# Kernel tuning notes

Hardware: AMD Instinct MI355X
Metric: run time of the kernel (lower is better)

## Reference

```python
import jax, jax.numpy as jnp
import numpy as np

N_NODES = 100000
N_EDGES = 1600000
F_IN = 64
HIDDEN = 128
N_GRAPHS = 1024
EPS = 1e-5  # BatchNorm1d eps


def setup_inputs() -> dict:
    key = jax.random.key(0)
    ks = jax.random.split(key, 16)
    inp = {
        "x": jax.random.normal(ks[0], (N_NODES, F_IN), jnp.float32),
        "edge_index": jax.random.randint(ks[1], (2, N_EDGES), 0, N_NODES, dtype=jnp.int32),
        "edge_attr": jax.random.uniform(ks[2], (N_EDGES, 1), jnp.float32),
        "batch": jnp.sort(jax.random.randint(ks[3], (N_NODES,), 0, N_GRAPHS, dtype=jnp.int32)),
    }
    dims = [F_IN, HIDDEN, HIDDEN]
    for i in range(3):
        d_in = dims[i]
        kk = jax.random.split(ks[4 + i], 2)
        s = 1.0 / np.sqrt(d_in).astype(np.float32)
        inp[f"rel_w{i}"] = jax.random.uniform(kk[0], (d_in, HIDDEN), jnp.float32, -s, s)
        inp[f"rel_b{i}"] = jnp.zeros((HIDDEN,), jnp.float32)
        inp[f"root_w{i}"] = jax.random.uniform(kk[1], (d_in, HIDDEN), jnp.float32, -s, s)
        inp[f"bn_g{i}"] = jnp.ones((HIDDEN,), jnp.float32)
        inp[f"bn_b{i}"] = jnp.zeros((HIDDEN,), jnp.float32)
        inp[f"bn_m{i}"] = jnp.zeros((HIDDEN,), jnp.float32)
        inp[f"bn_v{i}"] = jnp.ones((HIDDEN,), jnp.float32)
    inp["head_w1"] = jax.random.uniform(ks[8], (HIDDEN, HIDDEN // 2), jnp.float32, -0.1, 0.1)
    inp["head_b1"] = jnp.zeros((HIDDEN // 2,), jnp.float32)
    inp["head_w2"] = jax.random.uniform(ks[9], (HIDDEN // 2, 1), jnp.float32, -0.1, 0.1)
    inp["head_b2"] = jnp.zeros((1,), jnp.float32)
    return inp


def _graph_conv(h, src, dst, ew, w_rel, b_rel, w_root):
    # PyG GraphConv (aggr='add'): lin_rel(sum_j e_ji * x_j) + lin_root(x_i)
    msg = h[src] * ew[:, None]                                   # [E, in] gather
    agg = jax.ops.segment_sum(msg, dst, num_segments=h.shape[0])  # [N, in] scatter-add
    return agg @ w_rel + b_rel + h @ w_root


def reference(x, edge_index, edge_attr, batch,
              rel_w0, rel_b0, root_w0, bn_g0, bn_b0, bn_m0, bn_v0,
              rel_w1, rel_b1, root_w1, bn_g1, bn_b1, bn_m1, bn_v1,
              rel_w2, rel_b2, root_w2, bn_g2, bn_b2, bn_m2, bn_v2,
              head_w1, head_b1, head_w2, head_b2):
    src, dst = edge_index[0], edge_index[1]
    ew = edge_attr[:, 0]
    layers = [
        (rel_w0, rel_b0, root_w0, bn_g0, bn_b0, bn_m0, bn_v0),
        (rel_w1, rel_b1, root_w1, bn_g1, bn_b1, bn_m1, bn_v1),
        (rel_w2, rel_b2, root_w2, bn_g2, bn_b2, bn_m2, bn_v2),
    ]
    h = x
    for (wr, br, wo, g, b, m, v) in layers:
        h = _graph_conv(h, src, dst, ew, wr, br, wo)
        # BatchNorm1d in eval mode (running stats) + ReLU; dropout is identity in eval
        h = jax.nn.relu((h - m) * (g * jax.lax.rsqrt(v + EPS)) + b)
    # global_mean_pool over graph assignment ids
    sums = jax.ops.segment_sum(h, batch, num_segments=N_GRAPHS)                       # [G, H]
    cnts = jax.ops.segment_sum(jnp.ones((h.shape[0],), h.dtype), batch, num_segments=N_GRAPHS)
    pooled = sums / jnp.maximum(cnts, 1.0)[:, None]
    hid = jax.nn.relu(pooled @ head_w1 + head_b1)
    out = hid @ head_w2 + head_b2
    return out[:, 0]
```

## Files before the change

### kernel.cpp

```cpp
#include <hip/hip_runtime.h>

#define N_NODES 100000
#define N_EDGES 1600000
#define F_IN 64
#define HIDDEN 128
#define N_GRAPHS 1024
#define EPS 1e-5f

typedef short short8 __attribute__((ext_vector_type(8)));
typedef float f32x4 __attribute__((ext_vector_type(4)));
typedef unsigned int uint;
typedef unsigned short ushort;

__device__ __forceinline__ ushort f2b(float f) {
    uint x = __float_as_uint(f);
    return (ushort)((x + 0x7fffu + ((x >> 16) & 1u)) >> 16);
}
__device__ __forceinline__ uint pack2(float a, float b) {
    return (uint)f2b(a) | ((uint)f2b(b) << 16);
}
__device__ __forceinline__ float b2f_lo(uint u) { return __uint_as_float(u << 16); }
__device__ __forceinline__ float b2f_hi(uint u) { return __uint_as_float(u & 0xffff0000u); }

#define NBLK_A 128
#define CHUNK ((N_EDGES + NBLK_A - 1) / NBLK_A)
#define BUCK_SHIFT 9
#define NBUCK ((N_NODES + 511) / 512)
#define SCAN_M (NBUCK * NBLK_A)
#define SCAN_T ((SCAN_M + 1023) / 1024)


__global__ __launch_bounds__(256) void bin_count_kernel(const int* __restrict__ ei,
                                                        int* __restrict__ counts) {
    __shared__ int cnt[NBUCK];
    int blk = blockIdx.x, t = threadIdx.x;
    for (int i = t; i < NBUCK; i += 256) cnt[i] = 0;
    __syncthreads();
    int e0 = blk * CHUNK, e1 = min(e0 + CHUNK, N_EDGES);
    for (int e = e0 + t; e < e1; e += 256)
        atomicAdd(&cnt[ei[N_EDGES + e] >> BUCK_SHIFT], 1);
    __syncthreads();
    for (int i = t; i < NBUCK; i += 256) counts[i * NBLK_A + blk] = cnt[i];
}

__global__ __launch_bounds__(1024) void sc_reduce_kernel(const int* __restrict__ counts,
                                                         int* __restrict__ partial) {
    __shared__ int lds[16];
    int b = blockIdx.x, t = threadIdx.x;
    int i = b * 1024 + t;
    int v = (i < SCAN_M) ? counts[i] : 0;
    #pragma unroll
    for (int off = 32; off > 0; off >>= 1) v += __shfl_down(v, off);
    if ((t & 63) == 0) lds[t >> 6] = v;
    __syncthreads();
    if (t == 0) {
        int s = 0;
        #pragma unroll
        for (int j = 0; j < 16; ++j) s += lds[j];
        partial[b] = s;
    }
}

__global__ __launch_bounds__(64) void sc_small_kernel(int* __restrict__ partial,
                                                      int* __restrict__ rowptr) {
    if (threadIdx.x == 0) {
        int s = 0;
        for (int j = 0; j < SCAN_T; ++j) { int v = partial[j]; partial[j] = s; s += v; }
        rowptr[N_NODES] = N_EDGES;
    }
}

__global__ __launch_bounds__(1024) void sc_apply_kernel(int* __restrict__ counts,
                                                        const int* __restrict__ partial) {
    __shared__ int lds[1024];
    int b = blockIdx.x, t = threadIdx.x;
    int i = b * 1024 + t;
    int v = (i < SCAN_M) ? counts[i] : 0;
    lds[t] = v;
    __syncthreads();
    for (int off = 1; off < 1024; off <<= 1) {
        int x = (t >= off) ? lds[t - off] : 0;
        __syncthreads();
        lds[t] += x;
        __syncthreads();
    }
    if (i < SCAN_M) counts[i] = lds[t] - v + partial[b];
}

__global__ __launch_bounds__(256) void bin_scatter_kernel(const int* __restrict__ ei,
                                                          const float* __restrict__ ea,
                                                          const int* __restrict__ counts,
                                                          int2* __restrict__ emb) {
    __shared__ int cur[NBUCK];
    int blk = blockIdx.x, t = threadIdx.x;
    for (int i = t; i < NBUCK; i += 256) cur[i] = counts[i * NBLK_A + blk];
    __syncthreads();
    int e0 = blk * CHUNK, e1 = min(e0 + CHUNK, N_EDGES);
    for (int e = e0 + t; e < e1; e += 256) {
        int s = ei[e], d = ei[N_EDGES + e];
        uint y = ((uint)f2b(ea[e]) << 16) | (uint)(d & 511);
        int p = atomicAdd(&cur[d >> BUCK_SHIFT], 1);
        emb[p] = make_int2(s, (int)y);
    }
}

__global__ __launch_bounds__(1024) void bucket_build_kernel(const int* __restrict__ counts,
                                                            const int2* __restrict__ emb,
                                                            int* __restrict__ rowptr,
                                                            int2* __restrict__ em) {
    __shared__ int hist[512];
    __shared__ int cursor[512];
    int b = blockIdx.x, t = threadIdx.x;
    int beg = counts[b * NBLK_A];
    int end = (b + 1 < NBUCK) ? counts[(b + 1) * NBLK_A] : N_EDGES;
    int nbase = b << BUCK_SHIFT;
    int nnodes = min(512, N_NODES - nbase);

    if (t < 512) hist[t] = 0;
    __syncthreads();
    for (int e = beg + t; e < end; e += 1024)
        atomicAdd(&hist[(uint)emb[e].y & 511u], 1);
    __syncthreads();

    int v = (t < 512) ? hist[t] : 0;
    for (int off = 1; off < 512; off <<= 1) {
        int x = (t < 512 && t >= off) ? hist[t - off] : 0;
        __syncthreads();
        if (t < 512) hist[t] += x;
        __syncthreads();
    }
    if (t < 512) {
        int excl = hist[t] - v;
        cursor[t] = beg + excl;
        if (t < nnodes) rowptr[nbase + t] = beg + excl;
    }
    __syncthreads();

    for (int e = beg + t; e < end; e += 1024) {
        int2 m = emb[e];
        int p = atomicAdd(&cursor[(uint)m.y & 511u], 1);
        em[p] = make_int2(m.x, (int)((uint)m.y & 0xffff0000u));
    }
}


#define PREP_X   (N_NODES * 32)
#define PREP_W0  8192
#define PREP_W1  16384
#define PREP_W2  16384
#define PREP_PZ  (N_GRAPHS * HIDDEN)
#define PREP_TOT (PREP_X + PREP_W0 + PREP_W1 + PREP_W2 + PREP_PZ)

__device__ __forceinline__ void cvt_w_elem(const float* W0, const float* W1, int F,
                                           int idx, uint* out) {
    int K = 2 * F;
    int c  = idx / (K / 2);
    int k2 = (idx % (K / 2)) * 2;
    float f0 = (k2 < F) ? W0[k2 * 128 + c] : W1[(k2 - F) * 128 + c];
    float f1 = (k2 + 1 < F) ? W0[(k2 + 1) * 128 + c] : W1[(k2 + 1 - F) * 128 + c];
    out[idx] = pack2(f0, f1);
}

__global__ __launch_bounds__(256) void prep_kernel(const float* __restrict__ x, uint* __restrict__ xb,
                                                   const float* __restrict__ rw0, const float* __restrict__ ow0,
                                                   const float* __restrict__ rw1, const float* __restrict__ ow1,
                                                   const float* __restrict__ rw2, const float* __restrict__ ow2,
                                                   uint* __restrict__ wb0, uint* __restrict__ wb1,
                                                   uint* __restrict__ wb2, float* __restrict__ pooled) {
    int i = blockIdx.x * 256 + threadIdx.x;
    if (i < PREP_X) {
        float2 v = ((const float2*)x)[i];
        xb[i] = pack2(v.x, v.y);
        return;
    }
    i -= PREP_X;
    if (i < PREP_W0) { cvt_w_elem(rw0, ow0, 64, i, wb0); return; }
    i -= PREP_W0;
    if (i < PREP_W1) { cvt_w_elem(rw1, ow1, 128, i, wb1); return; }
    i -= PREP_W1;
    if (i < PREP_W2) { cvt_w_elem(rw2, ow2, 128, i, wb2); return; }
    i -= PREP_W2;
    if (i < PREP_PZ) pooled[i] = 0.f;
}


template <int F>
__global__ __launch_bounds__(256) void agg_kernel(const ushort* __restrict__ h,
                                                  const int* __restrict__ rowptr,
                                                  const int2* __restrict__ em,
                                                  ushort* __restrict__ agg) {
    int node = blockIdx.x * 4 + (threadIdx.x >> 6);
    int lane = threadIdx.x & 63;
    int g  = lane >> 4;
    int sl = lane & 15;
    int beg = rowptr[node], end = rowptr[node + 1];
    int e = beg;

    if (F == 128) {
        float acc[8] = {};
        for (; e + 8 <= end; e += 8) {
            int2 mA = em[e + g];
            int2 mB = em[e + 4 + g];
            uint4 vA = *(const uint4*)(h + (size_t)mA.x * 128 + sl * 8);
            uint4 vB = *(const uint4*)(h + (size_t)mB.x * 128 + sl * 8);
            float wA = __int_as_float(mA.y), wB = __int_as_float(mB.y);
            acc[0] = fmaf(b2f_lo(vA.x), wA, acc[0]);
            acc[1] = fmaf(b2f_hi(vA.x), wA, acc[1]);
            acc[2] = fmaf(b2f_lo(vA.y), wA, acc[2]);
            acc[3] = fmaf(b2f_hi(vA.y), wA, acc[3]);
            acc[4] = fmaf(b2f_lo(vA.z), wA, acc[4]);
            acc[5] = fmaf(b2f_hi(vA.z), wA, acc[5]);
            acc[6] = fmaf(b2f_lo(vA.w), wA, acc[6]);
            acc[7] = fmaf(b2f_hi(vA.w), wA, acc[7]);
            acc[0] = fmaf(b2f_lo(vB.x), wB, acc[0]);
            acc[1] = fmaf(b2f_hi(vB.x), wB, acc[1]);
            acc[2] = fmaf(b2f_lo(vB.y), wB, acc[2]);
            acc[3] = fmaf(b2f_hi(vB.y), wB, acc[3]);
            acc[4] = fmaf(b2f_lo(vB.z), wB, acc[4]);
            acc[5] = fmaf(b2f_hi(vB.z), wB, acc[5]);
            acc[6] = fmaf(b2f_lo(vB.w), wB, acc[6]);
            acc[7] = fmaf(b2f_hi(vB.w), wB, acc[7]);
        }
        for (; e < end; e += 4) {
            int ej = e + g;
            if (ej < end) {
                int2 m = em[ej];
                uint4 v = *(const uint4*)(h + (size_t)m.x * 128 + sl * 8);
                float w = __int_as_float(m.y);
                acc[0] = fmaf(b2f_lo(v.x), w, acc[0]);
                acc[1] = fmaf(b2f_hi(v.x), w, acc[1]);
                acc[2] = fmaf(b2f_lo(v.y), w, acc[2]);
                acc[3] = fmaf(b2f_hi(v.y), w, acc[3]);
                acc[4] = fmaf(b2f_lo(v.z), w, acc[4]);
                acc[5] = fmaf(b2f_hi(v.z), w, acc[5]);
                acc[6] = fmaf(b2f_lo(v.w), w, acc[6]);
                acc[7] = fmaf(b2f_hi(v.w), w, acc[7]);
            }
        }
        #pragma unroll
        for (int f = 0; f < 8; ++f) {
            acc[f] += __shfl_xor(acc[f], 16);
            acc[f] += __shfl_xor(acc[f], 32);
        }
        if (lane < 16) {
            uint4 o;
            o.x = pack2(acc[0], acc[1]);
            o.y = pack2(acc[2], acc[3]);
            o.z = pack2(acc[4], acc[5]);
            o.w = pack2(acc[6], acc[7]);
            *(uint4*)(agg + (size_t)node * 128 + sl * 8) = o;
        }
    } else {
        float acc[4] = {};
        for (; e + 8 <= end; e += 8) {
            int2 mA = em[e + g];
            int2 mB = em[e + 4 + g];
            uint2 vA = *(const uint2*)(h + (size_t)mA.x * 64 + sl * 4);
            uint2 vB = *(const uint2*)(h + (size_t)mB.x * 64 + sl * 4);
            float wA = __int_as_float(mA.y), wB = __int_as_float(mB.y);
            acc[0] = fmaf(b2f_lo(vA.x), wA, acc[0]);
            acc[1] = fmaf(b2f_hi(vA.x), wA, acc[1]);
            acc[2] = fmaf(b2f_lo(vA.y), wA, acc[2]);
            acc[3] = fmaf(b2f_hi(vA.y), wA, acc[3]);
            acc[0] = fmaf(b2f_lo(vB.x), wB, acc[0]);
            acc[1] = fmaf(b2f_hi(vB.x), wB, acc[1]);
            acc[2] = fmaf(b2f_lo(vB.y), wB, acc[2]);
            acc[3] = fmaf(b2f_hi(vB.y), wB, acc[3]);
        }
        for (; e < end; e += 4) {
            int ej = e + g;
            if (ej < end) {
                int2 m = em[ej];
                uint2 v = *(const uint2*)(h + (size_t)m.x * 64 + sl * 4);
                float w = __int_as_float(m.y);
                acc[0] = fmaf(b2f_lo(v.x), w, acc[0]);
                acc[1] = fmaf(b2f_hi(v.x), w, acc[1]);
                acc[2] = fmaf(b2f_lo(v.y), w, acc[2]);
                acc[3] = fmaf(b2f_hi(v.y), w, acc[3]);
            }
        }
        #pragma unroll
        for (int f = 0; f < 4; ++f) {
            acc[f] += __shfl_xor(acc[f], 16);
            acc[f] += __shfl_xor(acc[f], 32);
        }
        if (lane < 16) {
            uint2 o;
            o.x = pack2(acc[0], acc[1]);
            o.y = pack2(acc[2], acc[3]);
            *(uint2*)(agg + (size_t)node * 64 + sl * 4) = o;
        }
    }
}


template <int F>
__global__ __launch_bounds__(256, 2) void gemm_mfma(const ushort* __restrict__ A0,
                                                    const ushort* __restrict__ A1,
                                                    const ushort* __restrict__ Wb,
                                                    const float* __restrict__ bias,
                                                    const float* __restrict__ bng,
                                                    const float* __restrict__ bnb,
                                                    const float* __restrict__ bnm,
                                                    const float* __restrict__ bnv,
                                                    ushort* __restrict__ out) {
    constexpr int K = 2 * F;
    constexpr int LDW = K + 8;
    __shared__ ushort Wl[128 * LDW];

    int t = threadIdx.x;
    for (int idx = t; idx < 128 * (K / 8); idx += 256) {
        int c  = idx / (K / 8);
        int k8 = (idx % (K / 8)) * 8;
        *(short8*)&Wl[c * LDW + k8] = *(const short8*)&Wb[c * K + k8];
    }
    __syncthreads();

    int wave = t >> 6, lane = t & 63;
    int m = lane & 15, quad = lane >> 4;
    int r0 = blockIdx.x * 128 + wave * 32 + m;
    int r1 = r0 + 16;

    f32x4 acc0[8], acc1[8];
    #pragma unroll
    for (int i = 0; i < 8; ++i) { acc0[i] = (f32x4)(0.f); acc1[i] = (f32x4)(0.f); }

    auto loadA = [&](int row, int k0) -> short8 {
        short8 v = {};
        if (row < N_NODES)
            v = (k0 < F) ? *(const short8*)(A0 + (size_t)row * F + k0)
                         : *(const short8*)(A1 + (size_t)row * F + (k0 - F));
        return v;
    };

    short8 a0 = loadA(r0, quad * 8);
    short8 a1 = loadA(r1, quad * 8);
    for (int kc = 0; kc < K; kc += 32) {
        int k0 = kc + quad * 8;
        short8 na0 = {}, na1 = {};
        if (kc + 32 < K) {
            na0 = loadA(r0, k0 + 32);
            na1 = loadA(r1, k0 + 32);
        }
        #pragma unroll
        for (int ct = 0; ct < 8; ++ct) {
            short8 b = *(const short8*)&Wl[(ct * 16 + m) * LDW + k0];
            acc0[ct] = __builtin_amdgcn_mfma_f32_16x16x32_bf16(a0, b, acc0[ct], 0, 0, 0);
            acc1[ct] = __builtin_amdgcn_mfma_f32_16x16x32_bf16(a1, b, acc1[ct], 0, 0, 0);
        }
        a0 = na0; a1 = na1;
    }

    int rb0 = blockIdx.x * 128 + wave * 32 + quad * 4;
    #pragma unroll
    for (int ct = 0; ct < 8; ++ct) {
        int c = ct * 16 + m;
        float sc = bng[c] * rsqrtf(bnv[c] + EPS);
        float sh = bnb[c] - bnm[c] * sc;
        float bi = bias[c];
        #pragma unroll
        for (int reg = 0; reg < 4; ++reg) {
            int r = rb0 + reg;
            if (r < N_NODES) {
                float v = fmaxf(fmaf(acc0[ct][reg] + bi, sc, sh), 0.f);
                out[(size_t)r * 128 + c] = f2b(v);
            }
            int r2 = rb0 + 16 + reg;
            if (r2 < N_NODES) {
                float v = fmaxf(fmaf(acc1[ct][reg] + bi, sc, sh), 0.f);
                out[(size_t)r2 * 128 + c] = f2b(v);
            }
        }
    }
}


#define POOL_NODES 64
__global__ __launch_bounds__(256) void pool_kernel(const ushort* __restrict__ h,
                                                   const int* __restrict__ batch,
                                                   float* __restrict__ pooled) {
    __shared__ int gb[POOL_NODES];
    int b = blockIdx.x, t = threadIdx.x;
    int n0 = b * POOL_NODES;
    if (t < POOL_NODES) {
        int n = n0 + t;
        gb[t] = (n < N_NODES) ? batch[n] : -1;
    }
    __syncthreads();
    int f2 = t & 63;
    int q  = t >> 6;
    const uint* hp = (const uint*)h;
    float alo = 0.f, ahi = 0.f;
    int gcur = -1;
    for (int i = q; i < POOL_NODES; i += 4) {
        int n = n0 + i;
        if (n >= N_NODES) break;
        int g = gb[i];
        if (g != gcur) {
            if (gcur >= 0) {
                atomicAdd(&pooled[(size_t)gcur * 128 + f2 * 2], alo);
                atomicAdd(&pooled[(size_t)gcur * 128 + f2 * 2 + 1], ahi);
            }
            gcur = g;
            alo = 0.f; ahi = 0.f;
        }
        uint u = hp[(size_t)n * 64 + f2];
        alo += b2f_lo(u);
        ahi += b2f_hi(u);
    }
    if (gcur >= 0) {
        atomicAdd(&pooled[(size_t)gcur * 128 + f2 * 2], alo);
        atomicAdd(&pooled[(size_t)gcur * 128 + f2 * 2 + 1], ahi);
    }
}


__global__ __launch_bounds__(64) void head_kernel(const float* __restrict__ pooled,
                                                  const int* __restrict__ batch,
                                                  const float* __restrict__ w1,
                                                  const float* __restrict__ b1,
                                                  const float* __restrict__ w2,
                                                  const float* __restrict__ b2,
                                                  float* __restrict__ out) {
    int g = blockIdx.x;
    int j = threadIdx.x;
    int lo = 0, hi = N_NODES;
    while (lo < hi) { int m = (lo + hi) >> 1; if (batch[m] <  g) lo = m + 1; else hi = m; }
    int start = lo;
    lo = 0; hi = N_NODES;
    while (lo < hi) { int m = (lo + hi) >> 1; if (batch[m] <= g) lo = m + 1; else hi = m; }
    float inv = 1.0f / fmaxf((float)(lo - start), 1.0f);

    float acc = b1[j];
    #pragma unroll 4
    for (int k = 0; k < 128; ++k)
        acc = fmaf(pooled[(size_t)g * 128 + k] * inv, w1[k * 64 + j], acc);
    float prod = fmaxf(acc, 0.f) * w2[j];
    #pragma unroll
    for (int off = 32; off > 0; off >>= 1)
        prod += __shfl_down(prod, off);
    if (j == 0) out[g] = prod + b2[0];
}


extern "C" void kernel_launch(void* const* d_in, const int* in_sizes, int n_in,
                              void* d_out, int out_size, void* d_ws, size_t ws_size,
                              hipStream_t stream) {
    const float* x     = (const float*)d_in[0];
    const int*   ei    = (const int*)d_in[1];
    const float* ea    = (const float*)d_in[2];
    const int*   batch = (const int*)d_in[3];
    const float* rel_w[3]  = {(const float*)d_in[4],  (const float*)d_in[11], (const float*)d_in[18]};
    const float* rel_b[3]  = {(const float*)d_in[5],  (const float*)d_in[12], (const float*)d_in[19]};
    const float* root_w[3] = {(const float*)d_in[6],  (const float*)d_in[13], (const float*)d_in[20]};
    const float* bn_g[3]   = {(const float*)d_in[7],  (const float*)d_in[14], (const float*)d_in[21]};
    const float* bn_b[3]   = {(const float*)d_in[8],  (const float*)d_in[15], (const float*)d_in[22]};
    const float* bn_m[3]   = {(const float*)d_in[9],  (const float*)d_in[16], (const float*)d_in[23]};
    const float* bn_v[3]   = {(const float*)d_in[10], (const float*)d_in[17], (const float*)d_in[24]};
    const float* head_w1 = (const float*)d_in[25];
    const float* head_b1 = (const float*)d_in[26];
    const float* head_w2 = (const float*)d_in[27];
    const float* head_b2 = (const float*)d_in[28];
    float* out = (float*)d_out;

    char* ws = (char*)d_ws;
    int*    rowptr  = (int*)(ws + 0);
    int*    counts  = (int*)(ws + 401408);
    int*    partial = (int*)(ws + 503808);
    int2*   em      = (int2*)(ws + 524288);
    ushort* xb      = (ushort*)(ws + 13631488);
    ushort* h_a     = (ushort*)(ws + 26431488);
    ushort* h_b     = (ushort*)(ws + 52031488);
    ushort* aggb    = (ushort*)(ws + 77631488);
    float*  pooled  = (float*)(ws + 103231488);
    ushort* wb      = (ushort*)(ws + 103755776);
    int2*   emb = (int2*)(ws + 77631488);

    ushort* wb0 = wb;
    ushort* wb1 = wb + 16384;
    ushort* wb2 = wb + 49152;

    prep_kernel<<<(PREP_TOT + 255) / 256, 256, 0, stream>>>(
        x, (uint*)xb, rel_w[0], root_w[0], rel_w[1], root_w[1], rel_w[2], root_w[2],
        (uint*)wb0, (uint*)wb1, (uint*)wb2, pooled);

    bin_count_kernel<<<NBLK_A, 256, 0, stream>>>(ei, counts);
    sc_reduce_kernel<<<SCAN_T, 1024, 0, stream>>>(counts, partial);
    sc_small_kernel<<<1, 64, 0, stream>>>(partial, rowptr);
    sc_apply_kernel<<<SCAN_T, 1024, 0, stream>>>(counts, partial);
    bin_scatter_kernel<<<NBLK_A, 256, 0, stream>>>(ei, ea, counts, emb);
    bucket_build_kernel<<<NBUCK, 1024, 0, stream>>>(counts, emb, rowptr, em);

    const int AGG_BLOCKS  = N_NODES / 4;
    const int GEMM_BLOCKS = (N_NODES + 127) / 128;

    agg_kernel<64><<<AGG_BLOCKS, 256, 0, stream>>>(xb, rowptr, em, aggb);
    gemm_mfma<64><<<GEMM_BLOCKS, 256, 0, stream>>>(aggb, xb, wb0, rel_b[0],
                                                   bn_g[0], bn_b[0], bn_m[0], bn_v[0], h_a);
    agg_kernel<128><<<AGG_BLOCKS, 256, 0, stream>>>(h_a, rowptr, em, aggb);
    gemm_mfma<128><<<GEMM_BLOCKS, 256, 0, stream>>>(aggb, h_a, wb1, rel_b[1],
                                                    bn_g[1], bn_b[1], bn_m[1], bn_v[1], h_b);
    agg_kernel<128><<<AGG_BLOCKS, 256, 0, stream>>>(h_b, rowptr, em, aggb);
    gemm_mfma<128><<<GEMM_BLOCKS, 256, 0, stream>>>(aggb, h_b, wb2, rel_b[2],
                                                    bn_g[2], bn_b[2], bn_m[2], bn_v[2], h_a);

    pool_kernel<<<(N_NODES + POOL_NODES - 1) / POOL_NODES, 256, 0, stream>>>(h_a, batch, pooled);
    head_kernel<<<N_GRAPHS, 64, 0, stream>>>(pooled, batch, head_w1, head_b1, head_w2, head_b2, out);
}
```

Before: 490.1 us.

## Fuse prep with bin count, drop scan launch, halve GEMM weight LDS

Merges the bf16 conversion/prep kernel with the edge bucket counting kernel into one launch. Folds the single-thread partial scan into sc_apply, where each block sums the preceding partials. Splits the GEMM weight staging into two K-halves so the shared tile is half the size, and raises the occupancy hint to 4 blocks per SM. The aim is fewer launches and more resident GEMM blocks, at the cost of extra barriers and reloading weights twice per block.

Result: faster. 454.0 us (-7.4%).

```diff
diff --git a/kernel.cpp b/kernel.cpp
--- a/kernel.cpp
+++ b/kernel.cpp
@@ -30,18 +30,60 @@
 #define SCAN_T ((SCAN_M + 1023) / 1024)
 
 
-__global__ __launch_bounds__(256) void bin_count_kernel(const int* __restrict__ ei,
-                                                        int* __restrict__ counts) {
+#define PREP_X   (N_NODES * 32)
+#define PREP_W0  8192
+#define PREP_W1  16384
+#define PREP_W2  16384
+#define PREP_PZ  (N_GRAPHS * HIDDEN)
+#define PREP_TOT (PREP_X + PREP_W0 + PREP_W1 + PREP_W2 + PREP_PZ)
+
+__device__ __forceinline__ void cvt_w_elem(const float* W0, const float* W1, int F,
+                                           int idx, uint* out) {
+    int K = 2 * F;
+    int c  = idx / (K / 2);
+    int k2 = (idx % (K / 2)) * 2;
+    float f0 = (k2 < F) ? W0[k2 * 128 + c] : W1[(k2 - F) * 128 + c];
+    float f1 = (k2 + 1 < F) ? W0[(k2 + 1) * 128 + c] : W1[(k2 + 1 - F) * 128 + c];
+    out[idx] = pack2(f0, f1);
+}
+
+__global__ __launch_bounds__(256) void prep_count_kernel(
+        const float* __restrict__ x, uint* __restrict__ xb,
+        const float* __restrict__ rw0, const float* __restrict__ ow0,
+        const float* __restrict__ rw1, const float* __restrict__ ow1,
+        const float* __restrict__ rw2, const float* __restrict__ ow2,
+        uint* __restrict__ wb0, uint* __restrict__ wb1,
+        uint* __restrict__ wb2, float* __restrict__ pooled,
+        const int* __restrict__ ei, int* __restrict__ counts) {
     __shared__ int cnt[NBUCK];
-    int blk = blockIdx.x, t = threadIdx.x;
-    for (int i = t; i < NBUCK; i += 256) cnt[i] = 0;
-    __syncthreads();
-    int e0 = blk * CHUNK, e1 = min(e0 + CHUNK, N_EDGES);
-    for (int e = e0 + t; e < e1; e += 256)
-        atomicAdd(&cnt[ei[N_EDGES + e] >> BUCK_SHIFT], 1);
-    __syncthreads();
-    for (int i = t; i < NBUCK; i += 256) counts[i * NBLK_A + blk] = cnt[i];
-}
+    int t = threadIdx.x;
+    if (blockIdx.x < NBLK_A) {
+        int blk = blockIdx.x;
+        for (int i = t; i < NBUCK; i += 256) cnt[i] = 0;
+        __syncthreads();
+        int e0 = blk * CHUNK, e1 = min(e0 + CHUNK, N_EDGES);
+        for (int e = e0 + t; e < e1; e += 256)
+            atomicAdd(&cnt[ei[N_EDGES + e] >> BUCK_SHIFT], 1);
+        __syncthreads();
+        for (int i = t; i < NBUCK; i += 256) counts[i * NBLK_A + blk] = cnt[i];
+        return;
+    }
+    int i = (blockIdx.x - NBLK_A) * 256 + t;
+    if (i < PREP_X) {
+        float2 v = ((const float2*)x)[i];
+        xb[i] = pack2(v.x, v.y);
+        return;
+    }
+    i -= PREP_X;
+    if (i < PREP_W0) { cvt_w_elem(rw0, ow0, 64, i, wb0); return; }
+    i -= PREP_W0;
+    if (i < PREP_W1) { cvt_w_elem(rw1, ow1, 128, i, wb1); return; }
+    i -= PREP_W1;
+    if (i < PREP_W2) { cvt_w_elem(rw2, ow2, 128, i, wb2); return; }
+    i -= PREP_W2;
+    if (i < PREP_PZ) pooled[i] = 0.f;
+}
+
 
 __global__ __launch_bounds__(1024) void sc_reduce_kernel(const int* __restrict__ counts,
                                                          int* __restrict__ partial) {
@@ -61,19 +103,18 @@
     }
 }
 
-__global__ __launch_bounds__(64) void sc_small_kernel(int* __restrict__ partial,
-                                                      int* __restrict__ rowptr) {
-    if (threadIdx.x == 0) {
+__global__ __launch_bounds__(1024) void sc_apply_kernel(int* __restrict__ counts,
+                                                        const int* __restrict__ partial,
+                                                        int* __restrict__ rowptr) {
+    __shared__ int lds[1024];
+    __shared__ int base;
+    int b = blockIdx.x, t = threadIdx.x;
+    if (t == 0) {
         int s = 0;
-        for (int j = 0; j < SCAN_T; ++j) { int v = partial[j]; partial[j] = s; s += v; }
-        rowptr[N_NODES] = N_EDGES;
-    }
-}
-
-__global__ __launch_bounds__(1024) void sc_apply_kernel(int* __restrict__ counts,
-                                                        const int* __restrict__ partial) {
-    __shared__ int lds[1024];
-    int b = blockIdx.x, t = threadIdx.x;
+        for (int j = 0; j < b; ++j) s += partial[j];
+        base = s;
+        if (b == 0) rowptr[N_NODES] = N_EDGES;
+    }
     int i = b * 1024 + t;
     int v = (i < SCAN_M) ? counts[i] : 0;
     lds[t] = v;
@@ -84,7 +125,7 @@
         lds[t] += x;
         __syncthreads();
     }
-    if (i < SCAN_M) counts[i] = lds[t] - v + partial[b];
+    if (i < SCAN_M) counts[i] = lds[t] - v + base;
 }
 
 __global__ __launch_bounds__(256) void bin_scatter_kernel(const int* __restrict__ ei,
@@ -141,46 +182,6 @@
         int p = atomicAdd(&cursor[(uint)m.y & 511u], 1);
         em[p] = make_int2(m.x, (int)((uint)m.y & 0xffff0000u));
     }
-}
-
-
-#define PREP_X   (N_NODES * 32)
-#define PREP_W0  8192
-#define PREP_W1  16384
-#define PREP_W2  16384
-#define PREP_PZ  (N_GRAPHS * HIDDEN)
-#define PREP_TOT (PREP_X + PREP_W0 + PREP_W1 + PREP_W2 + PREP_PZ)
-
-__device__ __forceinline__ void cvt_w_elem(const float* W0, const float* W1, int F,
-                                           int idx, uint* out) {
-    int K = 2 * F;
-    int c  = idx / (K / 2);
-    int k2 = (idx % (K / 2)) * 2;
-    float f0 = (k2 < F) ? W0[k2 * 128 + c] : W1[(k2 - F) * 128 + c];
-    float f1 = (k2 + 1 < F) ? W0[(k2 + 1) * 128 + c] : W1[(k2 + 1 - F) * 128 + c];
-    out[idx] = pack2(f0, f1);
-}
-
-__global__ __launch_bounds__(256) void prep_kernel(const float* __restrict__ x, uint* __restrict__ xb,
-                                                   const float* __restrict__ rw0, const float* __restrict__ ow0,
-                                                   const float* __restrict__ rw1, const float* __restrict__ ow1,
-                                                   const float* __restrict__ rw2, const float* __restrict__ ow2,
-                                                   uint* __restrict__ wb0, uint* __restrict__ wb1,
-                                                   uint* __restrict__ wb2, float* __restrict__ pooled) {
-    int i = blockIdx.x * 256 + threadIdx.x;
-    if (i < PREP_X) {
-        float2 v = ((const float2*)x)[i];
-        xb[i] = pack2(v.x, v.y);
-        return;
-    }
-    i -= PREP_X;
-    if (i < PREP_W0) { cvt_w_elem(rw0, ow0, 64, i, wb0); return; }
-    i -= PREP_W0;
-    if (i < PREP_W1) { cvt_w_elem(rw1, ow1, 128, i, wb1); return; }
-    i -= PREP_W1;
-    if (i < PREP_W2) { cvt_w_elem(rw2, ow2, 128, i, wb2); return; }
-    i -= PREP_W2;
-    if (i < PREP_PZ) pooled[i] = 0.f;
 }
 
 
@@ -295,7 +296,7 @@
 
 
 template <int F>
-__global__ __launch_bounds__(256, 2) void gemm_mfma(const ushort* __restrict__ A0,
+__global__ __launch_bounds__(256, 4) void gemm_mfma(const ushort* __restrict__ A0,
                                                     const ushort* __restrict__ A1,
                                                     const ushort* __restrict__ Wb,
                                                     const float* __restrict__ bias,
@@ -305,17 +306,10 @@
                                                     const float* __restrict__ bnv,
                                                     ushort* __restrict__ out) {
     constexpr int K = 2 * F;
-    constexpr int LDW = K + 8;
+    constexpr int LDW = F + 8;
     __shared__ ushort Wl[128 * LDW];
 
     int t = threadIdx.x;
-    for (int idx = t; idx < 128 * (K / 8); idx += 256) {
-        int c  = idx / (K / 8);
-        int k8 = (idx % (K / 8)) * 8;
-        *(short8*)&Wl[c * LDW + k8] = *(const short8*)&Wb[c * K + k8];
-    }
-    __syncthreads();
-
     int wave = t >> 6, lane = t & 63;
     int m = lane & 15, quad = lane >> 4;
     int r0 = blockIdx.x * 128 + wave * 32 + m;
@@ -325,30 +319,40 @@
     #pragma unroll
     for (int i = 0; i < 8; ++i) { acc0[i] = (f32x4)(0.f); acc1[i] = (f32x4)(0.f); }
 
-    auto loadA = [&](int row, int k0) -> short8 {
-        short8 v = {};
-        if (row < N_NODES)
-            v = (k0 < F) ? *(const short8*)(A0 + (size_t)row * F + k0)
-                         : *(const short8*)(A1 + (size_t)row * F + (k0 - F));
-        return v;
-    };
-
-    short8 a0 = loadA(r0, quad * 8);
-    short8 a1 = loadA(r1, quad * 8);
-    for (int kc = 0; kc < K; kc += 32) {
-        int k0 = kc + quad * 8;
-        short8 na0 = {}, na1 = {};
-        if (kc + 32 < K) {
-            na0 = loadA(r0, k0 + 32);
-            na1 = loadA(r1, k0 + 32);
-        }
-        #pragma unroll
-        for (int ct = 0; ct < 8; ++ct) {
-            short8 b = *(const short8*)&Wl[(ct * 16 + m) * LDW + k0];
-            acc0[ct] = __builtin_amdgcn_mfma_f32_16x16x32_bf16(a0, b, acc0[ct], 0, 0, 0);
-            acc1[ct] = __builtin_amdgcn_mfma_f32_16x16x32_bf16(a1, b, acc1[ct], 0, 0, 0);
-        }
-        a0 = na0; a1 = na1;
+    #pragma unroll
+    for (int half = 0; half < 2; ++half) {
+        const ushort* A = half ? A1 : A0;
+        for (int idx = t; idx < 128 * (F / 8); idx += 256) {
+            int c  = idx / (F / 8);
+            int k8 = (idx % (F / 8)) * 8;
+            *(short8*)&Wl[c * LDW + k8] = *(const short8*)&Wb[c * K + half * F + k8];
+        }
+        __syncthreads();
+
+        auto loadA = [&](int row, int k0) -> short8 {
+            short8 v = {};
+            if (row < N_NODES) v = *(const short8*)(A + (size_t)row * F + k0);
+            return v;
+        };
+
+        short8 a0 = loadA(r0, quad * 8);
+        short8 a1 = loadA(r1, quad * 8);
+        for (int kc = 0; kc < F; kc += 32) {
+            int k0 = kc + quad * 8;
+            short8 na0 = {}, na1 = {};
+            if (kc + 32 < F) {
+                na0 = loadA(r0, k0 + 32);
+                na1 = loadA(r1, k0 + 32);
+            }
+            #pragma unroll
+            for (int ct = 0; ct < 8; ++ct) {
+                short8 b = *(const short8*)&Wl[(ct * 16 + m) * LDW + k0];
+                acc0[ct] = __builtin_amdgcn_mfma_f32_16x16x32_bf16(a0, b, acc0[ct], 0, 0, 0);
+                acc1[ct] = __builtin_amdgcn_mfma_f32_16x16x32_bf16(a1, b, acc1[ct], 0, 0, 0);
+            }
+            a0 = na0; a1 = na1;
+        }
+        __syncthreads();
     }
 
     int rb0 = blockIdx.x * 128 + wave * 32 + quad * 4;
@@ -480,14 +484,13 @@
     ushort* wb1 = wb + 16384;
     ushort* wb2 = wb + 49152;
 
-    prep_kernel<<<(PREP_TOT + 255) / 256, 256, 0, stream>>>(
+    const int PREP_BLOCKS = NBLK_A + (PREP_TOT + 255) / 256;
+    prep_count_kernel<<<PREP_BLOCKS, 256, 0, stream>>>(
         x, (uint*)xb, rel_w[0], root_w[0], rel_w[1], root_w[1], rel_w[2], root_w[2],
-        (uint*)wb0, (uint*)wb1, (uint*)wb2, pooled);
-
-    bin_count_kernel<<<NBLK_A, 256, 0, stream>>>(ei, counts);
+        (uint*)wb0, (uint*)wb1, (uint*)wb2, pooled, ei, counts);
+
     sc_reduce_kernel<<<SCAN_T, 1024, 0, stream>>>(counts, partial);
-    sc_small_kernel<<<1, 64, 0, stream>>>(partial, rowptr);
-    sc_apply_kernel<<<SCAN_T, 1024, 0, stream>>>(counts, partial);
+    sc_apply_kernel<<<SCAN_T, 1024, 0, stream>>>(counts, partial, rowptr);
     bin_scatter_kernel<<<NBLK_A, 256, 0, stream>>>(ei, ea, counts, emb);
     bucket_build_kernel<<<NBUCK, 1024, 0, stream>>>(counts, emb, rowptr, em);
 
```
